# Optimization experiments

Measured on AMD Instinct MI355X. Metric: run time of the kernel, lower is better.

## Reference

```python
import jax, jax.numpy as jnp
import numpy as np
from jax import lax

EMBED = 512
HIDDEN = 1024
VOCAB = 50257
BATCH = 64


def setup_inputs() -> dict:
    key = jax.random.key(0)
    ks = jax.random.split(key, 7)
    s_ih = 1.0 / np.sqrt(HIDDEN)
    inp = {
        "features": jax.random.normal(ks[0], (BATCH, EMBED), dtype=jnp.float32),
        "W_ih": jax.random.uniform(ks[1], (4 * HIDDEN, EMBED), jnp.float32, -s_ih, s_ih),
        "W_hh": jax.random.uniform(ks[2], (4 * HIDDEN, HIDDEN), jnp.float32, -s_ih, s_ih),
        "b_ih": jax.random.uniform(ks[3], (4 * HIDDEN,), jnp.float32, -s_ih, s_ih),
        "b_hh": jax.random.uniform(ks[4], (4 * HIDDEN,), jnp.float32, -s_ih, s_ih),
        "W_fc": jax.random.uniform(ks[5], (VOCAB, HIDDEN), jnp.float32, -s_ih, s_ih),
        "b_fc": jax.random.uniform(ks[6], (VOCAB,), jnp.float32, -s_ih, s_ih),
        "max_seq_len": 18,
    }
    return inp


def reference(features, W_ih, W_hh, b_ih, b_hh, W_fc, b_fc, max_seq_len):
    # features: [B, E] fed at EVERY step (module re-feeds the same features).
    B = features.shape[0]
    H = W_hh.shape[1]
    # Input projection is constant across steps; hoist it (same math).
    x_proj = features @ W_ih.T + b_ih  # [B, 4H]

    def step(carry, _):
        h, c = carry
        gates = x_proj + h @ W_hh.T + b_hh  # [B, 4H], PyTorch gate order i,f,g,o
        i, f, g, o = jnp.split(gates, 4, axis=1)
        i = jax.nn.sigmoid(i)
        f = jax.nn.sigmoid(f)
        g = jnp.tanh(g)
        o = jax.nn.sigmoid(o)
        c_new = f * c + i * g
        h_new = o * jnp.tanh(c_new)
        out = h_new @ W_fc.T + b_fc  # [B, V]
        return (h_new, c_new), out

    h0 = jnp.zeros((B, H), dtype=features.dtype)
    c0 = jnp.zeros((B, H), dtype=features.dtype)
    _, outs = lax.scan(step, (h0, c0), None, length=max_seq_len)  # [T, B, V]
    return jnp.transpose(outs, (1, 0, 2))  # [B, T, V]
```

## Files before the change

### kernel.cpp

```cpp
#include <hip/hip_runtime.h>

#define EMBED  512
#define HIDDEN 1024
#define G4     4096
#define VOCAB  50257
#define BATCH  64
#define TSTEPS 18
#define MROWS  (BATCH*TSTEPS)

typedef __bf16 bf16x8 __attribute__((ext_vector_type(8)));
typedef __bf16 bf16x4 __attribute__((ext_vector_type(4)));
typedef float  f32x4  __attribute__((ext_vector_type(4)));

#define WS_HA_B   0
#define WS_HB_B   131072
#define WS_C_B    262144
#define WS_XB_B   524288
#define WS_HS_B   1572864
#define WS_WHH_B  3932160

__global__ __launch_bounds__(256) void k_init(float4* ws) {
    int i = blockIdx.x * blockDim.x + threadIdx.x;
    ws[i] = make_float4(0.f, 0.f, 0.f, 0.f);
}

__global__ __launch_bounds__(256) void k_cvt(const float* __restrict__ src,
                                             __bf16* __restrict__ dst) {
    int i = (blockIdx.x * blockDim.x + threadIdx.x) * 8;
    float4 a = *(const float4*)(src + i);
    float4 b = *(const float4*)(src + i + 4);
    bf16x8 v;
    v[0] = (__bf16)a.x; v[1] = (__bf16)a.y; v[2] = (__bf16)a.z; v[3] = (__bf16)a.w;
    v[4] = (__bf16)b.x; v[5] = (__bf16)b.y; v[6] = (__bf16)b.z; v[7] = (__bf16)b.w;
    *(bf16x8*)(dst + i) = v;
}

__global__ __launch_bounds__(256) void k_xproj(const float* __restrict__ feat,
                                               const float* __restrict__ W_ih,
                                               const float* __restrict__ b_ih,
                                               const float* __restrict__ b_hh,
                                               float* __restrict__ xb) {
    __shared__ float fsh[16][EMBED];
    const int tx = threadIdx.x;
    const int rc = blockIdx.x;
    const int b0 = blockIdx.y * 16;
    {
        int row = tx >> 4, seg = tx & 15;
        const float4* src = (const float4*)(feat + (b0 + row) * EMBED + seg * 32);
        float4* dst = (float4*)(&fsh[row][seg * 32]);
        #pragma unroll
        for (int c = 0; c < 8; ++c) dst[c] = src[c];
    }
    __syncthreads();
    const int jl = tx & 15, bl = tx >> 4;
    const int r = rc * 16 + jl;
    const int b = b0 + bl;
    const float4* w  = (const float4*)(W_ih + (size_t)r * EMBED);
    const float4* h4 = (const float4*)(&fsh[bl][0]);
    float acc = 0.f;
    #pragma unroll 4
    for (int k = 0; k < EMBED / 4; ++k) {
        float4 wv = w[k], hv = h4[k];
        acc += wv.x * hv.x + wv.y * hv.y + wv.z * hv.z + wv.w * hv.w;
    }
    xb[b * G4 + r] = acc + b_ih[r] + b_hh[r];
}

#define PJT 17

__global__ __launch_bounds__(256) void k_step(const __bf16* __restrict__ h_in,
                                              __bf16* __restrict__ h_out,
                                              float* __restrict__ c,
                                              const float* __restrict__ xb,
                                              const __bf16* __restrict__ Whh,
                                              __bf16* __restrict__ hs, int t) {
    __shared__ float part[16 * 64 * PJT];
    const int tx   = threadIdx.x;
    const int wave = tx >> 6;
    const int lane = tx & 63;
    const int q    = lane >> 4;
    const int r    = lane & 15;
    const int j0   = blockIdx.x * 16;
    const int kb   = wave * 256;

    f32x4 acc[4][4];
    #pragma unroll
    for (int i = 0; i < 4; ++i)
        #pragma unroll
        for (int g = 0; g < 4; ++g)
            acc[i][g] = (f32x4){0.f, 0.f, 0.f, 0.f};

    const __bf16* aBase = h_in + (size_t)r * HIDDEN + kb + q * 8;
    const __bf16* bBase = Whh + (size_t)(j0 + r) * HIDDEN + kb + q * 8;

    #pragma unroll 2
    for (int s = 0; s < 8; ++s) {
        const int ko = s * 32;
        bf16x8 av[4], bv[4];
        #pragma unroll
        for (int i = 0; i < 4; ++i)
            av[i] = *(const bf16x8*)(aBase + (size_t)i * 16 * HIDDEN + ko);
        #pragma unroll
        for (int g = 0; g < 4; ++g)
            bv[g] = *(const bf16x8*)(bBase + (size_t)g * 1024 * HIDDEN + ko);
        #pragma unroll
        for (int i = 0; i < 4; ++i)
            #pragma unroll
            for (int g = 0; g < 4; ++g)
                acc[i][g] = __builtin_amdgcn_mfma_f32_16x16x32_bf16(av[i], bv[g], acc[i][g], 0, 0, 0);
    }

    #pragma unroll
    for (int i = 0; i < 4; ++i)
        #pragma unroll
        for (int g = 0; g < 4; ++g)
            #pragma unroll
            for (int reg = 0; reg < 4; ++reg)
                part[((wave * 4 + g) * 64 + i * 16 + q * 4 + reg) * PJT + r] = acc[i][g][reg];
    __syncthreads();

    const int jl = tx & 15;
    const int m0 = tx >> 4;
    #pragma unroll
    for (int mi = 0; mi < 4; ++mi) {
        const int m = mi * 16 + m0;
        float gsum[4];
        #pragma unroll
        for (int g = 0; g < 4; ++g) {
            float s = xb[m * G4 + g * 1024 + j0 + jl];
            #pragma unroll
            for (int w = 0; w < 4; ++w)
                s += part[((w * 4 + g) * 64 + m) * PJT + jl];
            gsum[g] = s;
        }
        const float i_ = 1.f / (1.f + expf(-gsum[0]));
        const float f_ = 1.f / (1.f + expf(-gsum[1]));
        const float g_ = tanhf(gsum[2]);
        const float o_ = 1.f / (1.f + expf(-gsum[3]));
        const int ci = m * HIDDEN + j0 + jl;
        const float cn = f_ * c[ci] + i_ * g_;
        c[ci] = cn;
        const float hn = o_ * tanhf(cn);
        const __bf16 hb = (__bf16)hn;
        h_out[ci] = hb;
        hs[(size_t)(m * TSTEPS + t) * HIDDEN + j0 + jl] = hb;
    }
}

__device__ inline bf16x8 cvt2bf8(float4 a, float4 b) {
    bf16x8 v;
    v[0] = (__bf16)a.x; v[1] = (__bf16)a.y; v[2] = (__bf16)a.z; v[3] = (__bf16)a.w;
    v[4] = (__bf16)b.x; v[5] = (__bf16)b.y; v[6] = (__bf16)b.z; v[7] = (__bf16)b.w;
    return v;
}

#define LPITCH 40
#define NBLK 393
#define MBLK 9

__global__ __launch_bounds__(256) void k_fc(const __bf16* __restrict__ hs,
                                            const float* __restrict__ W_fc,
                                            const float* __restrict__ b_fc,
                                            float* __restrict__ out) {
    __shared__ __bf16 Ash[128 * LPITCH];
    __shared__ __bf16 Bsh[128 * LPITCH];
    const int tx = threadIdx.x;
    const int bid = blockIdx.x;
    const int mb = (bid % MBLK) * 128;
    const int nb = (bid / MBLK) * 128;

    const int srow = tx >> 1;
    const int half = tx & 1;
    const __bf16* aSrc = hs + (size_t)(mb + srow) * HIDDEN + half * 16;
    const int nclamp = min(nb + srow, VOCAB - 1);
    const float4* bSrc = (const float4*)(W_fc + (size_t)nclamp * HIDDEN + half * 16);
    __bf16* aDst = &Ash[srow * LPITCH + half * 16];
    __bf16* bDst = &Bsh[srow * LPITCH + half * 16];

    const int lane = tx & 63;
    const int wave = tx >> 6;
    const int q = lane >> 4;
    const int r = lane & 15;
    const int wm = (wave >> 1) * 64;
    const int wn = (wave & 1) * 64;

    const __bf16* aF[4];
    const __bf16* bF[4];
    #pragma unroll
    for (int i = 0; i < 4; ++i) aF[i] = &Ash[(wm + i * 16 + r) * LPITCH + q * 8];
    #pragma unroll
    for (int j = 0; j < 4; ++j) bF[j] = &Bsh[(wn + j * 16 + r) * LPITCH + q * 8];

    f32x4 acc[4][4];
    #pragma unroll
    for (int i = 0; i < 4; ++i)
        #pragma unroll
        for (int j = 0; j < 4; ++j)
            acc[i][j] = (f32x4){0.f, 0.f, 0.f, 0.f};

    bf16x8 a0p = *(const bf16x8*)aSrc;
    bf16x8 a1p = *(const bf16x8*)(aSrc + 8);
    float4 f0p = bSrc[0], f1p = bSrc[1], f2p = bSrc[2], f3p = bSrc[3];
    aSrc += 32; bSrc += 8;

    for (int k0 = 0; k0 < HIDDEN; k0 += 32) {
        *(bf16x8*)aDst = a0p;
        *(bf16x8*)(aDst + 8) = a1p;
        *(bf16x8*)bDst = cvt2bf8(f0p, f1p);
        *(bf16x8*)(bDst + 8) = cvt2bf8(f2p, f3p);
        __syncthreads();
        if (k0 + 32 < HIDDEN) {
            a0p = *(const bf16x8*)aSrc;
            a1p = *(const bf16x8*)(aSrc + 8);
            f0p = bSrc[0]; f1p = bSrc[1]; f2p = bSrc[2]; f3p = bSrc[3];
            aSrc += 32; bSrc += 8;
        }
        bf16x8 av[4], bv[4];
        #pragma unroll
        for (int i = 0; i < 4; ++i) av[i] = *(const bf16x8*)aF[i];
        #pragma unroll
        for (int j = 0; j < 4; ++j) bv[j] = *(const bf16x8*)bF[j];
        #pragma unroll
        for (int i = 0; i < 4; ++i)
            #pragma unroll
            for (int j = 0; j < 4; ++j)
                acc[i][j] = __builtin_amdgcn_mfma_f32_16x16x32_bf16(av[i], bv[j], acc[i][j], 0, 0, 0);
        __syncthreads();
    }

    #pragma unroll
    for (int j = 0; j < 4; ++j) {
        const int v = nb + wn + j * 16 + r;
        if (v < VOCAB) {
            const float bias = b_fc[v];
            #pragma unroll
            for (int i = 0; i < 4; ++i) {
                const int m0 = mb + wm + i * 16 + q * 4;
                float* op = out + (size_t)m0 * VOCAB + v;
                op[0]                 = acc[i][j][0] + bias;
                op[(size_t)VOCAB]     = acc[i][j][1] + bias;
                op[(size_t)VOCAB * 2] = acc[i][j][2] + bias;
                op[(size_t)VOCAB * 3] = acc[i][j][3] + bias;
            }
        }
    }
}

extern "C" void kernel_launch(void* const* d_in, const int* in_sizes, int n_in,
                              void* d_out, int out_size, void* d_ws, size_t ws_size,
                              hipStream_t stream) {
    const float* feat = (const float*)d_in[0];
    const float* W_ih = (const float*)d_in[1];
    const float* W_hh = (const float*)d_in[2];
    const float* b_ih = (const float*)d_in[3];
    const float* b_hh = (const float*)d_in[4];
    const float* W_fc = (const float*)d_in[5];
    const float* b_fc = (const float*)d_in[6];
    float* out = (float*)d_out;

    char* wsb = (char*)d_ws;
    __bf16* hA  = (__bf16*)(wsb + WS_HA_B);
    __bf16* hB  = (__bf16*)(wsb + WS_HB_B);
    float*  c   = (float*)(wsb + WS_C_B);
    float*  xb  = (float*)(wsb + WS_XB_B);
    __bf16* hs  = (__bf16*)(wsb + WS_HS_B);
    __bf16* Whh = (__bf16*)(wsb + WS_WHH_B);

    k_init<<<128, 256, 0, stream>>>((float4*)wsb);
    k_cvt<<<2048, 256, 0, stream>>>(W_hh, Whh);
    k_xproj<<<dim3(256, 4), 256, 0, stream>>>(feat, W_ih, b_ih, b_hh, xb);
    for (int t = 0; t < TSTEPS; ++t) {
        const __bf16* hi = (t & 1) ? hB : hA;
        __bf16*       ho = (t & 1) ? hA : hB;
        k_step<<<64, 256, 0, stream>>>(hi, ho, c, xb, Whh, hs, t);
    }
    k_fc<<<NBLK * MBLK, 256, 0, stream>>>(hs, W_fc, b_fc, out);
}
```

Baseline: 954.2 us.

## Fuse LSTM time steps into one persistent cooperative kernel with register-resident weights

Replaces the 18 per-step kernel launches, the W_hh conversion kernel and the init kernel with a single cooperative kernel. Each block keeps its bf16 slice of W_hh in registers and its cell state and input projection in registers, and steps are separated by grid-wide syncs. The first step skips the h@W_hh matmul because h0 is zero. Separately, the FC kernel's block index is remapped so that consecutive tiles land on the same XCD for better L2 locality. The cost is heavy register pressure and reliance on grid sync, with the old multi-kernel path kept as a fallback if the cooperative launch fails.

New measurement: 990.2 us. 1.04x slower.

```diff
diff --git a/kernel.cpp b/kernel.cpp
--- a/kernel.cpp
+++ b/kernel.cpp
@@ -1,4 +1,7 @@
 #include <hip/hip_runtime.h>
+#include <hip/hip_cooperative_groups.h>
+
+namespace cg = cooperative_groups;
 
 #define EMBED  512
 #define HIDDEN 1024
@@ -9,7 +12,6 @@
 #define MROWS  (BATCH*TSTEPS)
 
 typedef __bf16 bf16x8 __attribute__((ext_vector_type(8)));
-typedef __bf16 bf16x4 __attribute__((ext_vector_type(4)));
 typedef float  f32x4  __attribute__((ext_vector_type(4)));
 
 #define WS_HA_B   0
@@ -19,6 +21,13 @@
 #define WS_HS_B   1572864
 #define WS_WHH_B  3932160
 
+__device__ inline bf16x8 cvt2bf8(float4 a, float4 b) {
+    bf16x8 v;
+    v[0] = (__bf16)a.x; v[1] = (__bf16)a.y; v[2] = (__bf16)a.z; v[3] = (__bf16)a.w;
+    v[4] = (__bf16)b.x; v[5] = (__bf16)b.y; v[6] = (__bf16)b.z; v[7] = (__bf16)b.w;
+    return v;
+}
+
 __global__ __launch_bounds__(256) void k_init(float4* ws) {
     int i = blockIdx.x * blockDim.x + threadIdx.x;
     ws[i] = make_float4(0.f, 0.f, 0.f, 0.f);
@@ -29,10 +38,7 @@
     int i = (blockIdx.x * blockDim.x + threadIdx.x) * 8;
     float4 a = *(const float4*)(src + i);
     float4 b = *(const float4*)(src + i + 4);
-    bf16x8 v;
-    v[0] = (__bf16)a.x; v[1] = (__bf16)a.y; v[2] = (__bf16)a.z; v[3] = (__bf16)a.w;
-    v[4] = (__bf16)b.x; v[5] = (__bf16)b.y; v[6] = (__bf16)b.z; v[7] = (__bf16)b.w;
-    *(bf16x8*)(dst + i) = v;
+    *(bf16x8*)(dst + i) = cvt2bf8(a, b);
 }
 
 __global__ __launch_bounds__(256) void k_xproj(const float* __restrict__ feat,
@@ -67,6 +73,124 @@
 }
 
 #define PJT 17
+
+__global__ __launch_bounds__(256, 1) void k_lstm(const float* __restrict__ xb,
+                                                 const float* __restrict__ Whh32,
+                                                 __bf16* __restrict__ hA,
+                                                 __bf16* __restrict__ hB,
+                                                 __bf16* __restrict__ hs) {
+    __shared__ float part[16 * 64 * PJT];
+    const int tx   = threadIdx.x;
+    const int wave = tx >> 6;
+    const int lane = tx & 63;
+    const int q    = lane >> 4;
+    const int r    = lane & 15;
+    const int j0   = blockIdx.x * 16;
+    const int kb   = wave * 256;
+
+    bf16x8 bB[4][8];
+    {
+        const float* bsrc = Whh32 + (size_t)(j0 + r) * HIDDEN + kb + q * 8;
+        #pragma unroll
+        for (int g = 0; g < 4; ++g)
+            #pragma unroll
+            for (int s = 0; s < 8; ++s) {
+                const float4* p = (const float4*)(bsrc + (size_t)g * 1024 * HIDDEN + s * 32);
+                bB[g][s] = cvt2bf8(p[0], p[1]);
+            }
+    }
+
+    const int jl = tx & 15;
+    const int m0 = tx >> 4;
+    float cr[4];
+    float xbr[4][4];
+    #pragma unroll
+    for (int mi = 0; mi < 4; ++mi) {
+        cr[mi] = 0.f;
+        const int m = mi * 16 + m0;
+        #pragma unroll
+        for (int g = 0; g < 4; ++g)
+            xbr[mi][g] = xb[m * G4 + g * 1024 + j0 + jl];
+    }
+
+    cg::grid_group grid = cg::this_grid();
+
+    #pragma unroll
+    for (int mi = 0; mi < 4; ++mi) {
+        const int m = mi * 16 + m0;
+        const float i_ = 1.f / (1.f + expf(-xbr[mi][0]));
+        const float g_ = tanhf(xbr[mi][2]);
+        const float o_ = 1.f / (1.f + expf(-xbr[mi][3]));
+        const float cn = i_ * g_;
+        cr[mi] = cn;
+        const float hn = o_ * tanhf(cn);
+        const __bf16 hb = (__bf16)hn;
+        hB[m * HIDDEN + j0 + jl] = hb;
+        hs[(size_t)(m * TSTEPS + 0) * HIDDEN + j0 + jl] = hb;
+    }
+
+    #pragma unroll 1
+    for (int t = 1; t < TSTEPS; ++t) {
+        grid.sync();
+        const __bf16* hi = (t & 1) ? hB : hA;
+        __bf16*       ho = (t & 1) ? hA : hB;
+
+        f32x4 acc[4][4];
+        #pragma unroll
+        for (int i = 0; i < 4; ++i)
+            #pragma unroll
+            for (int g = 0; g < 4; ++g)
+                acc[i][g] = (f32x4){0.f, 0.f, 0.f, 0.f};
+
+        const __bf16* aBase = hi + (size_t)r * HIDDEN + kb + q * 8;
+        #pragma unroll
+        for (int s = 0; s < 8; ++s) {
+            const int ko = s * 32;
+            bf16x8 av[4];
+            #pragma unroll
+            for (int i = 0; i < 4; ++i)
+                av[i] = *(const bf16x8*)(aBase + (size_t)i * 16 * HIDDEN + ko);
+            #pragma unroll
+            for (int i = 0; i < 4; ++i)
+                #pragma unroll
+                for (int g = 0; g < 4; ++g)
+                    acc[i][g] = __builtin_amdgcn_mfma_f32_16x16x32_bf16(av[i], bB[g][s], acc[i][g], 0, 0, 0);
+        }
+
+        #pragma unroll
+        for (int i = 0; i < 4; ++i)
+            #pragma unroll
+            for (int g = 0; g < 4; ++g)
+                #pragma unroll
+                for (int reg = 0; reg < 4; ++reg)
+                    part[((wave * 4 + g) * 64 + i * 16 + q * 4 + reg) * PJT + r] = acc[i][g][reg];
+        __syncthreads();
+
+        #pragma unroll
+        for (int mi = 0; mi < 4; ++mi) {
+            const int m = mi * 16 + m0;
+            float gsum[4];
+            #pragma unroll
+            for (int g = 0; g < 4; ++g) {
+                float s = xbr[mi][g];
+                #pragma unroll
+                for (int w = 0; w < 4; ++w)
+                    s += part[((w * 4 + g) * 64 + m) * PJT + jl];
+                gsum[g] = s;
+            }
+            const float i_ = 1.f / (1.f + expf(-gsum[0]));
+            const float f_ = 1.f / (1.f + expf(-gsum[1]));
+            const float g_ = tanhf(gsum[2]);
+            const float o_ = 1.f / (1.f + expf(-gsum[3]));
+            const float cn = f_ * cr[mi] + i_ * g_;
+            cr[mi] = cn;
+            const float hn = o_ * tanhf(cn);
+            const __bf16 hb = (__bf16)hn;
+            ho[m * HIDDEN + j0 + jl] = hb;
+            hs[(size_t)(m * TSTEPS + t) * HIDDEN + j0 + jl] = hb;
+        }
+    }
+}
 
 __global__ __launch_bounds__(256) void k_step(const __bf16* __restrict__ h_in,
                                               __bf16* __restrict__ h_out,
@@ -147,16 +271,12 @@
     }
 }
 
-__device__ inline bf16x8 cvt2bf8(float4 a, float4 b) {
-    bf16x8 v;
-    v[0] = (__bf16)a.x; v[1] = (__bf16)a.y; v[2] = (__bf16)a.z; v[3] = (__bf16)a.w;
-    v[4] = (__bf16)b.x; v[5] = (__bf16)b.y; v[6] = (__bf16)b.z; v[7] = (__bf16)b.w;
-    return v;
-}
-
 #define LPITCH 40
 #define NBLK 393
 #define MBLK 9
+#define NWG  (NBLK*MBLK)
+#define XQ   (NWG/8)
+#define XR   (NWG%8)
 
 __global__ __launch_bounds__(256) void k_fc(const __bf16* __restrict__ hs,
                                             const float* __restrict__ W_fc,
@@ -166,8 +286,12 @@
     __shared__ __bf16 Bsh[128 * LPITCH];
     const int tx = threadIdx.x;
     const int bid = blockIdx.x;
-    const int mb = (bid % MBLK) * 128;
-    const int nb = (bid / MBLK) * 128;
+    const int xcd = bid & 7;
+    const int lid = bid >> 3;
+    const int base = (xcd < XR) ? xcd * (XQ + 1) : XR * (XQ + 1) + (xcd - XR) * XQ;
+    const int virt = base + lid;
+    const int mb = (virt % MBLK) * 128;
+    const int nb = (virt / MBLK) * 128;
 
     const int srow = tx >> 1;
     const int half = tx & 1;
@@ -266,13 +390,25 @@
     __bf16* hs  = (__bf16*)(wsb + WS_HS_B);
     __bf16* Whh = (__bf16*)(wsb + WS_WHH_B);
 
-    k_init<<<128, 256, 0, stream>>>((float4*)wsb);
-    k_cvt<<<2048, 256, 0, stream>>>(W_hh, Whh);
     k_xproj<<<dim3(256, 4), 256, 0, stream>>>(feat, W_ih, b_ih, b_hh, xb);
-    for (int t = 0; t < TSTEPS; ++t) {
-        const __bf16* hi = (t & 1) ? hB : hA;
-        __bf16*       ho = (t & 1) ? hA : hB;
-        k_step<<<64, 256, 0, stream>>>(hi, ho, c, xb, Whh, hs, t);
-    }
-    k_fc<<<NBLK * MBLK, 256, 0, stream>>>(hs, W_fc, b_fc, out);
-}
+
+    const float* xb_p  = xb;
+    const float* whh_p = W_hh;
+    __bf16* hA_p = hA;
+    __bf16* hB_p = hB;
+    __bf16* hs_p = hs;
+    void* kargs[] = {(void*)&xb_p, (void*)&whh_p, (void*)&hA_p, (void*)&hB_p, (void*)&hs_p};
+    hipError_t cerr = hipLaunchCooperativeKernel((const void*)k_lstm, dim3(64), dim3(256),
+                                                 kargs, 0u, stream);
+    if (cerr != hipSuccess) {
+        k_init<<<128, 256, 0, stream>>>((float4*)wsb);
+        k_cvt<<<2048, 256, 0, stream>>>(W_hh, Whh);
+        for (int t = 0; t < TSTEPS; ++t) {
+            const __bf16* hi = (t & 1) ? hB : hA;
+            __bf16*       ho = (t & 1) ? hA : hB;
+            k_step<<<64, 256, 0, stream>>>(hi, ho, c, xb, Whh, hs, t);
+        }
+    }
+
+    k_fc<<<NWG, 256, 0, stream>>>(hs, W_fc, b_fc, out);
+}
```
